# Kernel optimization log

Hardware: AMD Instinct MI355X
Metric: run time of the kernel (lower is better)

Reference implementation:

```python
import jax, jax.numpy as jnp
import numpy as np

B, W, F = 64, 128, 64          # batch, window (node feat dim), n_features (nodes)
H, OUTW = 4, 128               # num_heads, out window size
NEG_SLOPE = 0.2                # LeakyReLU negative slope (alpha)


def setup_inputs() -> dict:
    key = jax.random.key(0)
    ks = jax.random.split(key, 6)
    scale_in = 1.0 / np.sqrt(W)
    scale_a = 1.0 / np.sqrt(OUTW)
    return {
        "x": jax.random.normal(ks[0], (B, W, F), dtype=jnp.float32),
        "W_src": jax.random.normal(ks[1], (H * OUTW, W), dtype=jnp.float32) * scale_in,
        "b_src": jnp.zeros((H * OUTW,), dtype=jnp.float32),
        "W_dst": jax.random.normal(ks[2], (H * OUTW, W), dtype=jnp.float32) * scale_in,
        "b_dst": jnp.zeros((H * OUTW,), dtype=jnp.float32),
        "attn": jax.random.normal(ks[3], (H, OUTW), dtype=jnp.float32) * scale_a,
    }


def reference(x, W_src, b_src, W_dst, b_dst, attn):
    # x: [B, W, F] -> node features nf: [B, F, W] (F nodes, W-dim features)
    nf = jnp.transpose(x, (0, 2, 1))
    b, f, w = nf.shape
    h, outw = attn.shape
    # GATv2 separate source/destination projections (share_weights=False)
    fs = (nf @ W_src.T + b_src).reshape(b, f, h, outw)  # [B, F, H, outW]
    fd = (nf @ W_dst.T + b_dst).reshape(b, f, h, outw)
    # additive score over complete graph with self-loops: e[b,i,j,h,d]
    s = fs[:, :, None, :, :] + fd[:, None, :, :, :]      # [B, src, dst, H, outW]
    e = jnp.where(s >= 0, s, NEG_SLOPE * s)              # LeakyReLU
    scores = jnp.einsum('bijhd,hd->bhij', e, attn)       # [B, H, src, dst]
    # edge softmax: normalize over incoming edges (sources) per destination
    a = jax.nn.softmax(scores, axis=2)
    # weighted scatter-sum aggregation at destinations
    out = jnp.einsum('bhij,bihd->bjhd', a, fs)           # [B, F, H, outW]
    out = out.mean(axis=2)                               # mean over heads -> [B, F, outW]
    return jnp.transpose(out, (0, 2, 1))                 # [B, outW, F]
```

## Files before the change

### kernel.cpp

```cpp
#include <hip/hip_runtime.h>
#include <math.h>

#define BB 64
#define WW 128
#define FF 64
#define HH 4
#define OW 128


struct GemmRegion {
    float wq[2 * 128 * 68];
};
struct AttnRegion {
    float fsl[FF * 132];
    float fdl[FF * 132];
    float stT[FF * 68];
    float st2[FF * 68];
    float A6[OW], B4[OW];
    float redm[4 * 64];
    float invl[64];
    float xfer[256 * 36];
};
union SMem { GemmRegion g; AttnRegion a; };

__global__ void __launch_bounds__(512)
__attribute__((amdgpu_waves_per_eu(2, 2)))
gat_fused(
    const float* __restrict__ x,
    const float* __restrict__ Wsrc,
    const float* __restrict__ bsrc,
    const float* __restrict__ Wdst,
    const float* __restrict__ bdst,
    const float* __restrict__ attn,
    float* __restrict__ out)
{
    __shared__ __align__(16) SMem sm;
    __shared__ float bl[2 * 128];

    const int bx = blockIdx.x;
    const int h  = bx & 3;
    const int b  = bx >> 2;
    const int t  = threadIdx.x;

    const int m  = t >> 8;
    const int ig = (t >> 4) & 15;
    const int dg = t & 15;
    const int i0 = ig * 4;

    if (t < 256) bl[t] = (t & 128 ? bdst : bsrc)[h * 128 + (t & 127)];

    const float* xb = x + (size_t)b * (WW * FF);

    float acc[4][8] = {};

    for (int kh = 0; kh < 2; ++kh) {
        if (kh) __syncthreads();
        #pragma unroll
        for (int p = 0; p < 8; ++p) {
            const int idx = p * 512 + t;
            const int mm = idx >> 11, d = (idx >> 4) & 127, q = idx & 15;
            *(float4*)&sm.g.wq[(mm * 128 + d) * 68 + q * 4] =
                *(const float4*)((mm ? Wdst : Wsrc)
                                 + (size_t)(h * 128 + d) * WW + kh * 64 + q * 4);
        }
        __syncthreads();

        const float* xk = xb + (size_t)(kh * 64) * FF + i0;
        #pragma unroll 1
        for (int k0 = 0; k0 < 64; k0 += 4) {
            float4 wv[8];
            #pragma unroll
            for (int e = 0; e < 8; ++e)
                wv[e] = *(const float4*)&sm.g.wq[(m * 128 + dg + 16 * e) * 68 + k0];
            #pragma unroll
            for (int kk = 0; kk < 4; ++kk) {
                const float4 xv = *(const float4*)(xk + (size_t)(k0 + kk) * FF);
                #pragma unroll
                for (int e = 0; e < 8; ++e) {
                    const float wf = ((const float*)&wv[e])[kk];
                    acc[0][e] = fmaf(xv.x, wf, acc[0][e]);
                    acc[1][e] = fmaf(xv.y, wf, acc[1][e]);
                    acc[2][e] = fmaf(xv.z, wf, acc[2][e]);
                    acc[3][e] = fmaf(xv.w, wf, acc[3][e]);
                }
            }
        }
    }
    __syncthreads();

    {
        float* dst = m ? sm.a.fdl : sm.a.fsl;
        #pragma unroll
        for (int e = 0; e < 8; ++e) {
            const int d = dg + 16 * e;
            const float bv = bl[m * 128 + d];
            #pragma unroll
            for (int ii = 0; ii < 4; ++ii)
                dst[(i0 + ii) * 132 + d] = acc[ii][e] + bv;
        }
    }
    if (t < 128) {
        const float av = attn[h * OW + t];
        sm.a.A6[t] = 0.6f * av;
        sm.a.B4[t] = 0.4f * av;
    }
    __syncthreads();

    if (t < 256) {
        const int i = t & 63, sel = t >> 6;
        const float* src = (sel < 2 ? sm.a.fsl : sm.a.fdl) + i * 132 + (sel & 1) * 64;
        const float* a6  = sm.a.A6 + (sel & 1) * 64;
        float s = 0.0f;
        #pragma unroll
        for (int c = 0; c < 16; ++c) {
            float4 fv = *(const float4*)&src[c * 4];
            float4 av = *(const float4*)&a6[c * 4];
            s = fmaf(fv.x, av.x, fmaf(fv.y, av.y, fmaf(fv.z, av.z, fmaf(fv.w, av.w, s))));
        }
        sm.a.redm[sel * 64 + i] = s;
    }
    __syncthreads();

    {
        const int dh  = t >> 8;
        const int rem = t & 255;
        const int iT  = rem & 15;
        const int j0D = (rem >> 4) * 4;
        float4 scq[4];
        scq[0] = scq[1] = scq[2] = scq[3] = float4{0.f, 0.f, 0.f, 0.f};
        const int cBase = dh * 16;
        #pragma unroll 4
        for (int c = 0; c < 16; ++c) {
            const int dd0 = (cBase + c) * 4;
            const float4 b4 = *(const float4*)&sm.a.B4[dd0];
            float4 fdv[4];
            #pragma unroll
            for (int jj = 0; jj < 4; ++jj)
                fdv[jj] = *(const float4*)&sm.a.fdl[(j0D + jj) * 132 + dd0];
            #pragma unroll
            for (int ii = 0; ii < 4; ++ii) {
                const float4 fsv =
                    *(const float4*)&sm.a.fsl[(iT + 16 * ii) * 132 + dd0];
                float* sc = (float*)&scq[ii];
                #pragma unroll
                for (int jj = 0; jj < 4; ++jj) {
                    float r = sc[jj];
                    r = fmaf(b4.x, fabsf(fsv.x + fdv[jj].x), r);
                    r = fmaf(b4.y, fabsf(fsv.y + fdv[jj].y), r);
                    r = fmaf(b4.z, fabsf(fsv.z + fdv[jj].z), r);
                    r = fmaf(b4.w, fabsf(fsv.w + fdv[jj].w), r);
                    sc[jj] = r;
                }
            }
        }
        if (dh) {
            #pragma unroll
            for (int ii = 0; ii < 4; ++ii)
                *(float4*)&sm.a.st2[(iT + 16 * ii) * 68 + j0D] = scq[ii];
        }
        __syncthreads();
        if (!dh) {
            float cdj[4];
            #pragma unroll
            for (int jj = 0; jj < 4; ++jj)
                cdj[jj] = sm.a.redm[128 + j0D + jj] + sm.a.redm[192 + j0D + jj];
            #pragma unroll
            for (int ii = 0; ii < 4; ++ii) {
                const int i = iT + 16 * ii;
                const float4 p2 = *(const float4*)&sm.a.st2[i * 68 + j0D];
                const float csl = sm.a.redm[i] + sm.a.redm[64 + i];
                const float* sc = (const float*)&scq[ii];
                const float* pp = (const float*)&p2;
                #pragma unroll
                for (int jj = 0; jj < 4; ++jj)
                    sm.a.stT[(j0D + jj) * 68 + i] = sc[jj] + pp[jj] + csl + cdj[jj];
            }
        }
    }
    __syncthreads();

    if (t < 64) {
        const int j = t;
        float* row = &sm.a.stT[j * 68];
        float4 rv[16];
        float mx = -3.0e38f;
        #pragma unroll
        for (int q = 0; q < 16; ++q) {
            rv[q] = *(const float4*)&row[q * 4];
            mx = fmaxf(mx, fmaxf(fmaxf(rv[q].x, rv[q].y), fmaxf(rv[q].z, rv[q].w)));
        }
        float s = 0.0f;
        #pragma unroll
        for (int q = 0; q < 16; ++q) {
            float4 e;
            e.x = __expf(rv[q].x - mx);
            e.y = __expf(rv[q].y - mx);
            e.z = __expf(rv[q].z - mx);
            e.w = __expf(rv[q].w - mx);
            s += e.x + e.y + e.z + e.w;
            *(float4*)&row[q * 4] = e;
        }
        sm.a.invl[j] = 0.25f / s;
    }
    __syncthreads();

    {
        const int ih  = t >> 8;
        const int rem = t & 255;
        const int jT  = rem & 15;
        const int dgF = rem >> 4;
        const int dF  = dgF * 4;
        const int iBase = ih * 32;

        float ag[4][8] = {};
        #pragma unroll 2
        for (int i2 = 0; i2 < 32; i2 += 4) {
            float4 pq[4];
            #pragma unroll
            for (int jj = 0; jj < 4; ++jj)
                pq[jj] = *(const float4*)&sm.a.stT[(jT + 16 * jj) * 68 + iBase + i2];
            #pragma unroll
            for (int u = 0; u < 4; ++u) {
                const int i = iBase + i2 + u;
                const float4 f0 = *(const float4*)&sm.a.fsl[i * 132 + dF];
                const float4 f1 = *(const float4*)&sm.a.fsl[i * 132 + dF + 64];
                #pragma unroll
                for (int jj = 0; jj < 4; ++jj) {
                    const float p = ((const float*)&pq[jj])[u];
                    ag[jj][0] = fmaf(p, f0.x, ag[jj][0]);
                    ag[jj][1] = fmaf(p, f0.y, ag[jj][1]);
                    ag[jj][2] = fmaf(p, f0.z, ag[jj][2]);
                    ag[jj][3] = fmaf(p, f0.w, ag[jj][3]);
                    ag[jj][4] = fmaf(p, f1.x, ag[jj][4]);
                    ag[jj][5] = fmaf(p, f1.y, ag[jj][5]);
                    ag[jj][6] = fmaf(p, f1.z, ag[jj][6]);
                    ag[jj][7] = fmaf(p, f1.w, ag[jj][7]);
                }
            }
        }

        if (ih) {
            #pragma unroll
            for (int jj = 0; jj < 4; ++jj) {
                float4 a0 = {ag[jj][0], ag[jj][1], ag[jj][2], ag[jj][3]};
                float4 a1 = {ag[jj][4], ag[jj][5], ag[jj][6], ag[jj][7]};
                *(float4*)&sm.a.xfer[rem * 36 + jj * 8]     = a0;
                *(float4*)&sm.a.xfer[rem * 36 + jj * 8 + 4] = a1;
            }
        }
        __syncthreads();
        if (!ih) {
            float* ob = out + (size_t)b * OW * FF;
            #pragma unroll
            for (int jj = 0; jj < 4; ++jj) {
                const float4 a0 = *(const float4*)&sm.a.xfer[rem * 36 + jj * 8];
                const float4 a1 = *(const float4*)&sm.a.xfer[rem * 36 + jj * 8 + 4];
                const float iv = sm.a.invl[jT + 16 * jj];
                const int j = jT + 16 * jj;
                atomicAdd(ob + (size_t)(dF + 0) * FF + j, (ag[jj][0] + a0.x) * iv);
                atomicAdd(ob + (size_t)(dF + 1) * FF + j, (ag[jj][1] + a0.y) * iv);
                atomicAdd(ob + (size_t)(dF + 2) * FF + j, (ag[jj][2] + a0.z) * iv);
                atomicAdd(ob + (size_t)(dF + 3) * FF + j, (ag[jj][3] + a0.w) * iv);
                atomicAdd(ob + (size_t)(dF + 64) * FF + j, (ag[jj][4] + a1.x) * iv);
                atomicAdd(ob + (size_t)(dF + 65) * FF + j, (ag[jj][5] + a1.y) * iv);
                atomicAdd(ob + (size_t)(dF + 66) * FF + j, (ag[jj][6] + a1.z) * iv);
                atomicAdd(ob + (size_t)(dF + 67) * FF + j, (ag[jj][7] + a1.w) * iv);
            }
        }
    }
}

extern "C" void kernel_launch(void* const* d_in, const int* in_sizes, int n_in,
                              void* d_out, int out_size, void* d_ws, size_t ws_size,
                              hipStream_t stream) {
    const float* x    = (const float*)d_in[0];
    const float* Wsrc = (const float*)d_in[1];
    const float* bsrc = (const float*)d_in[2];
    const float* Wdst = (const float*)d_in[3];
    const float* bdst = (const float*)d_in[4];
    const float* attn = (const float*)d_in[5];

    hipMemsetAsync(d_out, 0, (size_t)out_size, stream);
    gat_fused<<<BB * HH, 512, 0, stream>>>(x, Wsrc, bsrc, Wdst, bdst, attn,
                                           (float*)d_out);
}
```

Measured before the change: 101.1 us.

## Stage full projection weights once and parallelize softmax across all threads

The projection GEMM now loads both K-halves of the source and destination weights into shared memory in one pass, dropping the second load phase and its barrier. The price is twice the shared-memory footprint for the GEMM region, which may reduce occupancy. The edge softmax is rewritten so each destination row is handled by 8 threads using xor-shuffle reductions instead of one thread per row over 64 elements, so all 512 threads do work instead of 64.

```diff
diff --git a/kernel.cpp b/kernel.cpp
--- a/kernel.cpp
+++ b/kernel.cpp
@@ -9,7 +9,7 @@
 
 
 struct GemmRegion {
-    float wq[2 * 128 * 68];
+    float wq[2 * 2 * 128 * 68];
 };
 struct AttnRegion {
     float fsl[FF * 132];
@@ -51,30 +51,33 @@
 
     const float* xb = x + (size_t)b * (WW * FF);
 
+    #pragma unroll
+    for (int p = 0; p < 16; ++p) {
+        const int idx = p * 512 + t;
+        const int kh = idx >> 12;
+        const int mm = (idx >> 11) & 1;
+        const int d  = (idx >> 4) & 127;
+        const int q  = idx & 15;
+        *(float4*)&sm.g.wq[((kh << 8) + mm * 128 + d) * 68 + q * 4] =
+            *(const float4*)((mm ? Wdst : Wsrc)
+                             + (size_t)(h * 128 + d) * WW + kh * 64 + q * 4);
+    }
+    __syncthreads();
+
     float acc[4][8] = {};
-
-    for (int kh = 0; kh < 2; ++kh) {
-        if (kh) __syncthreads();
-        #pragma unroll
-        for (int p = 0; p < 8; ++p) {
-            const int idx = p * 512 + t;
-            const int mm = idx >> 11, d = (idx >> 4) & 127, q = idx & 15;
-            *(float4*)&sm.g.wq[(mm * 128 + d) * 68 + q * 4] =
-                *(const float4*)((mm ? Wdst : Wsrc)
-                                 + (size_t)(h * 128 + d) * WW + kh * 64 + q * 4);
-        }
-        __syncthreads();
-
-        const float* xk = xb + (size_t)(kh * 64) * FF + i0;
-        #pragma unroll 1
-        for (int k0 = 0; k0 < 64; k0 += 4) {
+    {
+        const int wrow = m * 128 + dg;
+        #pragma unroll 2
+        for (int k0 = 0; k0 < 128; k0 += 4) {
+            const int kq = k0 >> 6;
+            const int kw = k0 & 63;
             float4 wv[8];
             #pragma unroll
             for (int e = 0; e < 8; ++e)
-                wv[e] = *(const float4*)&sm.g.wq[(m * 128 + dg + 16 * e) * 68 + k0];
+                wv[e] = *(const float4*)&sm.g.wq[((kq << 8) + wrow + 16 * e) * 68 + kw];
             #pragma unroll
             for (int kk = 0; kk < 4; ++kk) {
-                const float4 xv = *(const float4*)(xk + (size_t)(k0 + kk) * FF);
+                const float4 xv = *(const float4*)(xb + (size_t)(k0 + kk) * FF + i0);
                 #pragma unroll
                 for (int e = 0; e < 8; ++e) {
                     const float wf = ((const float*)&wv[e])[kk];
@@ -179,28 +182,27 @@
     }
     __syncthreads();
 
-    if (t < 64) {
-        const int j = t;
-        float* row = &sm.a.stT[j * 68];
-        float4 rv[16];
-        float mx = -3.0e38f;
-        #pragma unroll
-        for (int q = 0; q < 16; ++q) {
-            rv[q] = *(const float4*)&row[q * 4];
-            mx = fmaxf(mx, fmaxf(fmaxf(rv[q].x, rv[q].y), fmaxf(rv[q].z, rv[q].w)));
-        }
-        float s = 0.0f;
-        #pragma unroll
-        for (int q = 0; q < 16; ++q) {
-            float4 e;
-            e.x = __expf(rv[q].x - mx);
-            e.y = __expf(rv[q].y - mx);
-            e.z = __expf(rv[q].z - mx);
-            e.w = __expf(rv[q].w - mx);
-            s += e.x + e.y + e.z + e.w;
-            *(float4*)&row[q * 4] = e;
-        }
-        sm.a.invl[j] = 0.25f / s;
+    {
+        const int j   = t >> 3;
+        const int sub = t & 7;
+        float* rp = &sm.a.stT[j * 68 + sub * 8];
+        float4 r0 = *(const float4*)(rp);
+        float4 r1 = *(const float4*)(rp + 4);
+        float mx = fmaxf(fmaxf(fmaxf(r0.x, r0.y), fmaxf(r0.z, r0.w)),
+                         fmaxf(fmaxf(r1.x, r1.y), fmaxf(r1.z, r1.w)));
+        #pragma unroll
+        for (int o = 1; o < 8; o <<= 1) mx = fmaxf(mx, __shfl_xor(mx, o));
+        float4 e0, e1;
+        e0.x = __expf(r0.x - mx); e0.y = __expf(r0.y - mx);
+        e0.z = __expf(r0.z - mx); e0.w = __expf(r0.w - mx);
+        e1.x = __expf(r1.x - mx); e1.y = __expf(r1.y - mx);
+        e1.z = __expf(r1.z - mx); e1.w = __expf(r1.w - mx);
+        float s = e0.x + e0.y + e0.z + e0.w + e1.x + e1.y + e1.z + e1.w;
+        #pragma unroll
+        for (int o = 1; o < 8; o <<= 1) s += __shfl_xor(s, o);
+        *(float4*)(rp)     = e0;
+        *(float4*)(rp + 4) = e1;
+        if (sub == 0) sm.a.invl[j] = 0.25f / s;
     }
     __syncthreads();
 
```

Result: no change. 100.4 us, median of 2 (-0.7%).
